# Performance work log

Measured on AMD Instinct MI355X. Metric: run time of the kernel, lower is better.

## Reference

```python
import math
import jax, jax.numpy as jnp
import numpy as np

EMBED_DIM = 512
NUM_HEADS = 8
EDGE_VOC = 16
EDGE_PAD = 0
L, B = 512, 16


def setup_inputs() -> dict:
    key = jax.random.key(0)
    ks = jax.random.split(key, 8)
    x = jax.random.normal(ks[0], (L, B, EMBED_DIM), dtype=jnp.float32)
    edge = jax.random.randint(ks[1], (B, L, L), 0, EDGE_VOC, dtype=jnp.int32)
    key_padding_mask = jnp.zeros((B, L), dtype=bool)
    # causal additive mask, as from nn.Transformer.generate_square_subsequent_mask
    attn_mask = jnp.where(jnp.triu(jnp.ones((L, L), bool), k=1), -jnp.inf, 0.0).astype(jnp.float32)
    s = 1.0 / math.sqrt(EMBED_DIM)
    in_proj_w = jax.random.uniform(ks[2], (3 * EMBED_DIM, EMBED_DIM), jnp.float32, -s, s)
    in_proj_b = jnp.zeros((3 * EMBED_DIM,), jnp.float32)
    out_proj_w = jax.random.uniform(ks[3], (EMBED_DIM, EMBED_DIM), jnp.float32, -s, s)
    out_proj_b = jnp.zeros((EMBED_DIM,), jnp.float32)
    edge_emb = jax.random.normal(ks[4], (EDGE_VOC, NUM_HEADS), dtype=jnp.float32)
    edge_emb = edge_emb.at[EDGE_PAD].set(0.0)  # padding_idx row zeroed
    return {"x": x, "edge": edge, "key_padding_mask": key_padding_mask,
            "attn_mask": attn_mask, "in_proj_w": in_proj_w, "in_proj_b": in_proj_b,
            "out_proj_w": out_proj_w, "out_proj_b": out_proj_b, "edge_emb": edge_emb}


def reference(x, edge, key_padding_mask, attn_mask,
              in_proj_w, in_proj_b, out_proj_w, out_proj_b, edge_emb):
    length, bsz, embed_dim = x.shape
    H = edge_emb.shape[1]
    hd = embed_dim // H
    qkv = x @ in_proj_w.T + in_proj_b                       # (L, B, 3E)
    q, k, v = jnp.split(qkv, 3, axis=-1)
    # (L, B*H, hd) -> (B*H, L, hd)
    q = q.reshape(length, bsz * H, hd).transpose(1, 0, 2)
    k = k.reshape(length, bsz * H, hd).transpose(1, 0, 2)
    v = v.reshape(length, bsz * H, hd).transpose(1, 0, 2)
    # combine attn_mask with key padding
    mask = attn_mask[None]                                   # (1, L, L)
    kpm = jnp.broadcast_to(key_padding_mask[:, None, None, :],
                           (bsz, H, 1, length)).reshape(bsz * H, 1, length)
    mask = jnp.where(kpm, -jnp.inf, mask)                    # (B*H, 1/L, L)
    # edge bias: (B, L, L, H) -> (B*H, L, L)
    ebias = edge_emb[edge].transpose(0, 3, 1, 2).reshape(bsz * H, length, length)
    q = q / math.sqrt(hd)
    scores = jnp.einsum('bqd,bkd->bqk', q, k) + mask + ebias
    attn = jax.nn.softmax(scores, axis=-1)
    out = jnp.einsum('bqk,bkd->bqd', attn, v)                # (B*H, L, hd)
    out = out.transpose(1, 0, 2).reshape(length, bsz, embed_dim)
    return out @ out_proj_w.T + out_proj_b
```

## Files before the change

### kernel.cpp

```cpp
#include <hip/hip_runtime.h>
#include <hip/hip_bf16.h>


typedef __attribute__((ext_vector_type(8))) short bf16x8;
typedef __attribute__((ext_vector_type(4))) float f32x4;
typedef __attribute__((ext_vector_type(4))) int i32x4;

#define LOG2E 1.44269504088896340736f
#define QK_SCALE 0.18033688011112042f

__device__ inline void gll16(const void* g, const void* l) {
  __builtin_amdgcn_global_load_lds(
      (const __attribute__((address_space(1))) unsigned int*)g,
      (__attribute__((address_space(3))) unsigned int*)l, 16, 0, 0);
}

__device__ inline short f2bf(float x) {
  __hip_bfloat16 t = __float2bfloat16(x);
  return *reinterpret_cast<short*>(&t);
}

__device__ inline void cstore(__hip_bfloat16* C, size_t idx, float v) {
  C[idx] = __float2bfloat16(v);
}
__device__ inline void cstore(float* C, size_t idx, float v) { C[idx] = v; }

__global__ void cvt3(const float* __restrict__ x, const float* __restrict__ w1,
                     const float* __restrict__ w2, __hip_bfloat16* __restrict__ xb,
                     __hip_bfloat16* __restrict__ w1b,
                     __hip_bfloat16* __restrict__ w2b) {
  const int blk = blockIdx.x;
  const float* src;
  __hip_bfloat16* dst;
  int off;
  if (blk < 2048)      { src = x;  dst = xb;  off = blk; }
  else if (blk < 2432) { src = w1; dst = w1b; off = blk - 2048; }
  else                 { src = w2; dst = w2b; off = blk - 2432; }
  const int i = (off * 256 + threadIdx.x) * 8;
  const float4 a = *(const float4*)(src + i);
  const float4 b = *(const float4*)(src + i + 4);
  bf16x8 r;
  r[0] = f2bf(a.x); r[1] = f2bf(a.y); r[2] = f2bf(a.z); r[3] = f2bf(a.w);
  r[4] = f2bf(b.x); r[5] = f2bf(b.y); r[6] = f2bf(b.z); r[7] = f2bf(b.w);
  *(bf16x8*)(dst + i) = r;
}

template <int MT, int RB, typename TC, bool QS = false, bool BROW = false>
__global__ __launch_bounds__(256, RB) void gemm_bt(
    const __hip_bfloat16* __restrict__ A,
    const __hip_bfloat16* __restrict__ W,
    const float* __restrict__ bias,
    TC* __restrict__ C, int N, int K) {
  constexpr int MI = MT / 32;
  __shared__ short As[MT * 32];
  __shared__ short Ws[128 * 32];
  const int tid = threadIdx.x;
  const int wave = tid >> 6, lane = tid & 63;
  const int c = lane & 15, quad = lane >> 4;
  const int nb = N >> 7;
  const int bx = blockIdx.x % nb, by = blockIdx.x / nb;
  const int m0 = by * MT, n0 = bx << 7;
  const int wm = wave >> 1, wn = wave & 1;

  f32x4 acc[MI][4] = {};
  const int ar = lane >> 2;
  const int ak = (lane & 3) * 8;

  for (int k0 = 0; k0 < K; k0 += 32) {
    __syncthreads();
#pragma unroll
    for (int i = 0; i < MT / 64; i++) {
      const int r0 = i * 64 + wave * 16;
      gll16(A + (size_t)(m0 + r0 + ar) * K + k0 + ak, &As[r0 * 32]);
    }
#pragma unroll
    for (int i = 0; i < 2; i++) {
      const int r0 = i * 64 + wave * 16;
      gll16(W + (size_t)(n0 + r0 + ar) * K + k0 + ak, &Ws[r0 * 32]);
    }
    __syncthreads();
    bf16x8 af[MI], bfr[4];
#pragma unroll
    for (int i = 0; i < MI; i++)
      af[i] = *(const bf16x8*)&As[(wm * (MT / 2) + i * 16 + c) * 32 + quad * 8];
#pragma unroll
    for (int j = 0; j < 4; j++)
      bfr[j] = *(const bf16x8*)&Ws[(wn * 64 + j * 16 + c) * 32 + quad * 8];
#pragma unroll
    for (int i = 0; i < MI; i++)
#pragma unroll
      for (int j = 0; j < 4; j++)
        acc[i][j] = __builtin_amdgcn_mfma_f32_16x16x32_bf16(af[i], bfr[j],
                                                            acc[i][j], 0, 0, 0);
  }
#pragma unroll
  for (int j = 0; j < 4; j++) {
    const int col = n0 + wn * 64 + j * 16 + c;
    const float bv = bias[col];
#pragma unroll
    for (int i = 0; i < MI; i++) {
      const int row = m0 + wm * (MT / 2) + i * 16 + quad * 4;
#pragma unroll
      for (int r = 0; r < 4; r++) {
        float v = acc[i][j][r] + bv;
        if constexpr (QS) {
          if (col < 512) v *= QK_SCALE;
        }
        int orow = row + r;
        if constexpr (BROW) orow = ((orow & 15) << 9) | (orow >> 4);
        cstore(C, (size_t)orow * N + col, v);
      }
    }
  }
}

__global__ __launch_bounds__(256, 4) void attn_kernel(
    const __hip_bfloat16* __restrict__ qkv,
    const int* __restrict__ edge,
    const float* __restrict__ edge_emb,
    __hip_bfloat16* __restrict__ attn_out) {
  __shared__ short Ks[64 * 72];
  __shared__ short Vt[64 * 72];
  __shared__ short Ps[4][16 * 72];
  __shared__ float eeS[16];

  const int tid = threadIdx.x;
  const int wave = tid >> 6, lane = tid & 63;
  const int c = lane & 15, quad = lane >> 4;
  const int i = blockIdx.x;
  constexpr int pi[8] = {0, 7, 1, 6, 2, 5, 3, 4};
  const int xcd = i & 7;
  const int j = i >> 3;
  const int qb = pi[j & 7];
  const int h = (j >> 3) & 7;
  const int b = xcd + ((j >> 6) << 3);
  const int colq = h * 64;

  if (tid < 16) eeS[tid] = (edge_emb[tid * 8 + h] - 16.0f) * LOG2E;

  const int q_g = (qb << 6) + wave * 16 + c;
  bf16x8 qf0, qf1;
  {
    const __hip_bfloat16* qp_ = qkv + (size_t)(b * 512 + q_g) * 1536 + colq;
    qf0 = *(const bf16x8*)(qp_ + quad * 8);
    qf1 = *(const bf16x8*)(qp_ + 32 + quad * 8);
  }
  float lsum = 0.f;
  f32x4 o[4] = {};
  const int* erow = edge + ((size_t)(b * 512 + q_g)) * 512;

  const int r2 = tid >> 3;
  const int cc = (tid & 7) * 8;
  const int kcol0 = ((r2 << 1) & 7) | (((r2 >> 2) ^ (cc >> 3)) << 3);
  const size_t sbase0 = (size_t)(b * 512 + r2 * 2) * 1536 + colq + cc;
  bf16x8 kreg[2], vreg[2];
  kreg[0] = *(const bf16x8*)(qkv + sbase0 + 512);
  vreg[0] = *(const bf16x8*)(qkv + sbase0 + 1024);
  kreg[1] = *(const bf16x8*)(qkv + sbase0 + 1536 + 512);
  vreg[1] = *(const bf16x8*)(qkv + sbase0 + 1536 + 1024);

  __syncthreads();

  const int nkt = qb + 1;
  for (int kt = 0; kt < nkt; kt++) {
    const int k0 = kt << 6;
    const bool last = (kt == qb);
    const int mtmax = last ? (wave + 1) : 4;
    if (kt) __syncthreads();
    *(bf16x8*)&Ks[(r2 * 2) * 72 + cc] = kreg[0];
    *(bf16x8*)&Ks[(r2 * 2 + 1) * 72 + cc] = kreg[1];
#pragma unroll
    for (int j2 = 0; j2 < 8; j2++) {
      short2 p;
      p.x = vreg[0][j2];
      p.y = vreg[1][j2];
      *(short2*)&Vt[(cc + j2) * 72 + kcol0] = p;
    }
    if (kt + 1 < nkt) {
      const size_t nb_ = sbase0 + (size_t)(kt + 1) * 64 * 1536;
      kreg[0] = *(const bf16x8*)(qkv + nb_ + 512);
      vreg[0] = *(const bf16x8*)(qkv + nb_ + 1024);
      kreg[1] = *(const bf16x8*)(qkv + nb_ + 1536 + 512);
      vreg[1] = *(const bf16x8*)(qkv + nb_ + 1536 + 1024);
    }
    i32x4 e4[4];
#pragma unroll
    for (int mt = 0; mt < 4; mt++)
      if (mt < mtmax)
        e4[mt] = *(const i32x4*)(erow + k0 + mt * 16 + quad * 4);
    __syncthreads();

    f32x4 st[4];
    __builtin_amdgcn_s_setprio(1);
#pragma unroll
    for (int mt = 0; mt < 4; mt++) {
      if (mt >= mtmax) continue;
      f32x4 z;
#pragma unroll
      for (int r = 0; r < 4; r++) z[r] = eeS[e4[mt][r]];
      const bf16x8 ka = *(const bf16x8*)&Ks[(mt * 16 + c) * 72 + quad * 8];
      const bf16x8 kb = *(const bf16x8*)&Ks[(mt * 16 + c) * 72 + 32 + quad * 8];
      z = __builtin_amdgcn_mfma_f32_16x16x32_bf16(ka, qf0, z, 0, 0, 0);
      st[mt] = __builtin_amdgcn_mfma_f32_16x16x32_bf16(kb, qf1, z, 0, 0, 0);
    }
    __builtin_amdgcn_s_setprio(0);

    float rs[4] = {0.f, 0.f, 0.f, 0.f};
#pragma unroll
    for (int mt = 0; mt < 4; mt++) {
      short4 pk = {0, 0, 0, 0};
      if (mt < mtmax) {
        if (last && mt == wave) {
#pragma unroll
          for (int r = 0; r < 4; r++) {
            const float p = (quad * 4 + r <= c) ? exp2f(st[mt][r]) : 0.0f;
            rs[r] += p;
            ((short*)&pk)[r] = f2bf(p);
          }
        } else {
#pragma unroll
          for (int r = 0; r < 4; r++) {
            const float p = exp2f(st[mt][r]);
            rs[r] += p;
            ((short*)&pk)[r] = f2bf(p);
          }
        }
      }
      *(short4*)&Ps[wave][c * 72 + mt * 16 + quad * 4] = pk;
    }
    lsum += (rs[0] + rs[1]) + (rs[2] + rs[3]);

    const bool skip_hi = last && (wave < 2);
    const bf16x8 pa0 = *(const bf16x8*)&Ps[wave][c * 72 + quad * 8];
    bf16x8 pa1;
    if (!skip_hi) pa1 = *(const bf16x8*)&Ps[wave][c * 72 + 32 + quad * 8];
    __builtin_amdgcn_s_setprio(1);
#pragma unroll
    for (int nt = 0; nt < 4; nt++) {
      const int n = nt * 16 + c;
      const bf16x8 vb0 = *(const bf16x8*)&Vt[n * 72 + ((quad ^ (n >> 3)) << 3)];
      o[nt] = __builtin_amdgcn_mfma_f32_16x16x32_bf16(pa0, vb0, o[nt], 0, 0, 0);
      if (!skip_hi) {
        const bf16x8 vb1 =
            *(const bf16x8*)&Vt[n * 72 + (((4 + quad) ^ (n >> 3)) << 3)];
        o[nt] = __builtin_amdgcn_mfma_f32_16x16x32_bf16(pa1, vb1, o[nt], 0, 0, 0);
      }
    }
    __builtin_amdgcn_s_setprio(0);
  }

  float l = lsum;
  l += __shfl_xor(l, 16);
  l += __shfl_xor(l, 32);
  float lr[4];
#pragma unroll
  for (int r = 0; r < 4; r++) lr[r] = __shfl(l, quad * 4 + r, 16);
  const int qrow0 = (qb << 6) + wave * 16 + quad * 4;
#pragma unroll
  for (int nt = 0; nt < 4; nt++)
#pragma unroll
    for (int r = 0; r < 4; r++)
      attn_out[(size_t)((qrow0 + r) * 16 + b) * 512 + colq + nt * 16 + c] =
          __float2bfloat16(o[nt][r] / lr[r]);
}

extern "C" void kernel_launch(void* const* d_in, const int* in_sizes, int n_in,
                              void* d_out, int out_size, void* d_ws, size_t ws_size,
                              hipStream_t stream) {
  const float* x    = (const float*)d_in[0];
  const int* edge   = (const int*)d_in[1];
  const float* ipw  = (const float*)d_in[4];
  const float* ipb  = (const float*)d_in[5];
  const float* opw  = (const float*)d_in[6];
  const float* opb  = (const float*)d_in[7];
  const float* eemb = (const float*)d_in[8];
  float* out = (float*)d_out;

  __hip_bfloat16* qkv  = (__hip_bfloat16*)d_ws;
  __hip_bfloat16* attn = qkv + (size_t)8192 * 1536;
  __hip_bfloat16* xb   = attn + (size_t)8192 * 512;
  __hip_bfloat16* w1b  = xb + (size_t)8192 * 512;
  __hip_bfloat16* w2b  = w1b + (size_t)1536 * 512;

  cvt3<<<2560, 256, 0, stream>>>(x, ipw, opw, xb, w1b, w2b);
  gemm_bt<128, 3, __hip_bfloat16, true, true>
      <<<768, 256, 0, stream>>>(xb, w1b, ipb, qkv, 1536, 512);
  attn_kernel<<<1024, 256, 0, stream>>>(qkv, edge, eemb, attn);
  gemm_bt<64, 2, float>
      <<<512, 256, 0, stream>>>(attn, w2b, opb, out, 512, 512);
}
```

Measured before the change: 151.6 us.

## Pre-pack edge indices to bytes in MFMA order and rebalance query-block mapping

Adds blocks to the conversion kernel that pack the int32 edge matrix into bytes, reordered to match the attention kernel's MFMA fragment layout. Attention then does one 16-byte load per key tile instead of four int32x4 loads, cutting its edge bandwidth and load count. The cost is an extra full read of the int32 edge tensor plus a packed write, even for masked-out causal regions. The query-block permutation is also rotated per block group to spread causal work across CUs.

```diff
diff --git a/kernel.cpp b/kernel.cpp
--- a/kernel.cpp
+++ b/kernel.cpp
@@ -26,17 +26,50 @@
 __device__ inline void cstore(float* C, size_t idx, float v) { C[idx] = v; }
 
 __global__ void cvt3(const float* __restrict__ x, const float* __restrict__ w1,
-                     const float* __restrict__ w2, __hip_bfloat16* __restrict__ xb,
+                     const float* __restrict__ w2, const int* __restrict__ edge,
+                     __hip_bfloat16* __restrict__ xb,
                      __hip_bfloat16* __restrict__ w1b,
-                     __hip_bfloat16* __restrict__ w2b) {
+                     __hip_bfloat16* __restrict__ w2b,
+                     unsigned char* __restrict__ epk) {
   const int blk = blockIdx.x;
+  const int tid = threadIdx.x;
+  if (blk >= 2560) {
+    __shared__ unsigned char Ls[4 * 512];
+    const int pblk = blk - 2560;
+    const int b = pblk >> 7;
+    const int q0 = (pblk & 127) * 4;
+    const int row = tid >> 6, lk = tid & 63;
+    const int k0 = lk * 8;
+    const int* src = edge + ((size_t)(b * 512 + q0 + row)) * 512 + k0;
+    const i32x4 a = *(const i32x4*)src;
+    const i32x4 b4 = *(const i32x4*)(src + 4);
+    const unsigned int lo =
+        (unsigned)a[0] | ((unsigned)a[1] << 8) | ((unsigned)a[2] << 16) |
+        ((unsigned)a[3] << 24);
+    const unsigned int hi =
+        (unsigned)b4[0] | ((unsigned)b4[1] << 8) | ((unsigned)b4[2] << 16) |
+        ((unsigned)b4[3] << 24);
+    const int kt = k0 >> 6, kk = k0 & 63;
+    const int mt = kk >> 4, quad = (kk >> 2) & 3;
+    const int doff = row * 512 + kt * 64 + quad * 16 + mt * 4;
+    *(unsigned int*)&Ls[doff] = lo;
+    *(unsigned int*)&Ls[doff + 16] = hi;
+    __syncthreads();
+    const int okt = tid >> 5, rowi = (tid >> 3) & 3, off8 = (tid & 7) * 8;
+    const unsigned long long v =
+        *(const unsigned long long*)&Ls[rowi * 512 + okt * 64 + off8];
+    *(unsigned long long*)&epk[(((size_t)(b * 8 + okt) * 512) + q0 + rowi) *
+                                   64 +
+                               off8] = v;
+    return;
+  }
   const float* src;
   __hip_bfloat16* dst;
   int off;
   if (blk < 2048)      { src = x;  dst = xb;  off = blk; }
   else if (blk < 2432) { src = w1; dst = w1b; off = blk - 2048; }
   else                 { src = w2; dst = w2b; off = blk - 2432; }
-  const int i = (off * 256 + threadIdx.x) * 8;
+  const int i = (off * 256 + tid) * 8;
   const float4 a = *(const float4*)(src + i);
   const float4 b = *(const float4*)(src + i + 4);
   bf16x8 r;
@@ -116,7 +149,7 @@
 
 __global__ __launch_bounds__(256, 4) void attn_kernel(
     const __hip_bfloat16* __restrict__ qkv,
-    const int* __restrict__ edge,
+    const unsigned char* __restrict__ epk,
     const float* __restrict__ edge_emb,
     __hip_bfloat16* __restrict__ attn_out) {
   __shared__ short Ks[64 * 72];
@@ -131,7 +164,7 @@
   constexpr int pi[8] = {0, 7, 1, 6, 2, 5, 3, 4};
   const int xcd = i & 7;
   const int j = i >> 3;
-  const int qb = pi[j & 7];
+  const int qb = pi[(j + (j >> 5)) & 7];
   const int h = (j >> 3) & 7;
   const int b = xcd + ((j >> 6) << 3);
   const int colq = h * 64;
@@ -147,7 +180,8 @@
   }
   float lsum = 0.f;
   f32x4 o[4] = {};
-  const int* erow = edge + ((size_t)(b * 512 + q_g)) * 512;
+  const unsigned char* eb =
+      epk + (((size_t)(b * 8) * 512 + q_g) << 6) + (quad << 4);
 
   const int r2 = tid >> 3;
   const int cc = (tid & 7) * 8;
@@ -163,7 +197,6 @@
 
   const int nkt = qb + 1;
   for (int kt = 0; kt < nkt; kt++) {
-    const int k0 = kt << 6;
     const bool last = (kt == qb);
     const int mtmax = last ? (wave + 1) : 4;
     if (kt) __syncthreads();
@@ -183,11 +216,7 @@
       kreg[1] = *(const bf16x8*)(qkv + nb_ + 1536 + 512);
       vreg[1] = *(const bf16x8*)(qkv + nb_ + 1536 + 1024);
     }
-    i32x4 e4[4];
-#pragma unroll
-    for (int mt = 0; mt < 4; mt++)
-      if (mt < mtmax)
-        e4[mt] = *(const i32x4*)(erow + k0 + mt * 16 + quad * 4);
+    const i32x4 e16 = *(const i32x4*)(eb + ((size_t)kt << 15));
     __syncthreads();
 
     f32x4 st[4];
@@ -195,9 +224,10 @@
 #pragma unroll
     for (int mt = 0; mt < 4; mt++) {
       if (mt >= mtmax) continue;
+      const unsigned int w = (unsigned int)e16[mt];
       f32x4 z;
 #pragma unroll
-      for (int r = 0; r < 4; r++) z[r] = eeS[e4[mt][r]];
+      for (int r = 0; r < 4; r++) z[r] = eeS[(w >> (8 * r)) & 15];
       const bf16x8 ka = *(const bf16x8*)&Ks[(mt * 16 + c) * 72 + quad * 8];
       const bf16x8 kb = *(const bf16x8*)&Ks[(mt * 16 + c) * 72 + 32 + quad * 8];
       z = __builtin_amdgcn_mfma_f32_16x16x32_bf16(ka, qf0, z, 0, 0, 0);
@@ -281,11 +311,12 @@
   __hip_bfloat16* xb   = attn + (size_t)8192 * 512;
   __hip_bfloat16* w1b  = xb + (size_t)8192 * 512;
   __hip_bfloat16* w2b  = w1b + (size_t)1536 * 512;
-
-  cvt3<<<2560, 256, 0, stream>>>(x, ipw, opw, xb, w1b, w2b);
+  unsigned char* epk = (unsigned char*)(w2b + (size_t)512 * 512);
+
+  cvt3<<<4608, 256, 0, stream>>>(x, ipw, opw, edge, xb, w1b, w2b, epk);
   gemm_bt<128, 3, __hip_bfloat16, true, true>
       <<<768, 256, 0, stream>>>(xb, w1b, ipb, qkv, 1536, 512);
-  attn_kernel<<<1024, 256, 0, stream>>>(qkv, edge, eemb, attn);
+  attn_kernel<<<1024, 256, 0, stream>>>(qkv, epk, eemb, attn);
   gemm_bt<64, 2, float>
       <<<512, 256, 0, stream>>>(attn, w2b, opb, out, 512, 512);
 }
```

Result: faster. 148.6 us (-2.0%).
